# Performance work log

Hardware: AMD Instinct MI355X
Metric: run time of the kernel (lower is better)

Reference implementation:

```python
import jax, jax.numpy as jnp
import numpy as np

N, M, D, H = 256, 1024, 512, 512


def setup_inputs() -> dict:
    key = jax.random.key(0)
    k1, k2, k3, k4 = jax.random.split(key, 4)
    scale = 1.0 / np.sqrt(D)
    return {
        "embeddings": jax.random.normal(k1, (N, D), dtype=jnp.float32),
        "support_tensors": jax.random.normal(k2, (M, D), dtype=jnp.float32),
        "W1": jax.random.normal(k3, (D, H), dtype=jnp.float32) * scale,
        "b1": jnp.zeros((H,), dtype=jnp.float32),
        "W2": jax.random.normal(k4, (H, 1), dtype=jnp.float32) * (1.0 / np.sqrt(H)),
        "b2": jnp.zeros((1,), dtype=jnp.float32),
    }


def reference(embeddings, support_tensors, W1, b1, W2, b2):
    # SupportLayer.call: tile queries x support set into all N*M pairs,
    # apply pairwise kernel (siamese head: sigmoid(MLP(|a - b|))),
    # reshape back to similarity matrix [N, M].
    # Broadcasting replaces the explicit tf.tile / reshape.
    diff = jnp.abs(embeddings[:, None, :] - support_tensors[None, :, :])  # [N, M, D]
    h = jax.nn.relu(jnp.einsum("nmd,dh->nmh", diff, W1) + b1)             # [N, M, H]
    logits = jnp.einsum("nmh,ho->nmo", h, W2)[..., 0] + b2[0]             # [N, M]
    return jax.nn.sigmoid(logits)
```

## Files before the change

kernel.cpp:

```cpp
#include <hip/hip_runtime.h>
#include <hip/hip_bf16.h>

#define N_Q 256
#define M_S 1024
#define DD 512
#define HH 512

typedef __attribute__((ext_vector_type(8))) short short8;
typedef __attribute__((ext_vector_type(8))) __bf16 bf16x8;
typedef __attribute__((ext_vector_type(16))) float f32x16;
typedef __attribute__((ext_vector_type(2))) __bf16 bf16x2;

union U8 { short8 s; bf16x8 b; };

__device__ __forceinline__ unsigned short f2bf(float f) {
  unsigned int u = __float_as_uint(f);
  u += 0x7FFFu + ((u >> 16) & 1u);
  return (unsigned short)(u >> 16);
}

__device__ __forceinline__ short8 pack8(const float* d) {
#if defined(__has_builtin) && __has_builtin(__builtin_amdgcn_cvt_pk_bf16_f32)
  short8 r;
#pragma unroll
  for (int i = 0; i < 4; ++i) {
    union { bf16x2 v; short s[2]; } u;
    u.v = __builtin_amdgcn_cvt_pk_bf16_f32(d[2 * i], d[2 * i + 1]);
    r[2 * i] = u.s[0];
    r[2 * i + 1] = u.s[1];
  }
  return r;
#else
  short8 r;
#pragma unroll
  for (int i = 0; i < 8; ++i) r[i] = (short)f2bf(d[i]);
  return r;
#endif
}

__device__ __forceinline__ short8 packdiff(float4 e0, float4 e1, float4 s0, float4 s1) {
  float d[8];
  d[0] = fabsf(e0.x - s0.x); d[1] = fabsf(e0.y - s0.y);
  d[2] = fabsf(e0.z - s0.z); d[3] = fabsf(e0.w - s0.w);
  d[4] = fabsf(e1.x - s1.x); d[5] = fabsf(e1.y - s1.y);
  d[6] = fabsf(e1.z - s1.z); d[7] = fabsf(e1.w - s1.w);
  return pack8(d);
}

__global__ __launch_bounds__(512) void prep_w1s(const float* __restrict__ W1,
                                                unsigned short* __restrict__ w1s) {
  const int f = blockIdx.x;
  const int kc = f >> 4, h32 = f & 15;
  const int l = threadIdx.x & 63, j = threadIdx.x >> 6;
  const int h = h32 * 32 + (l & 31);
  const int k = kc * 16 + (l >> 5) * 8 + j;
  w1s[f * 512 + l * 8 + j] = f2bf(W1[k * HH + h]);
}

__global__ __launch_bounds__(512, 4) void support_kernel(
    const float* __restrict__ emb, const float* __restrict__ sup,
    const unsigned short* __restrict__ w1s, const float* __restrict__ b1,
    const float* __restrict__ W2, const float* __restrict__ b2,
    float* __restrict__ out) {
  __shared__ short8 As16[64 * 64];

  const int tid = threadIdx.x;
  const int lane = tid & 63;
  const int wid = tid >> 6;
  const int l31 = lane & 31;
  const int khalf = lane >> 5;

  const int m0 = blockIdx.x * 16;
  const int n0 = blockIdx.y * 4;

  const int c = tid & 63;
  const int rg = tid >> 6;
  const int nl = rg >> 1;
  const int mq = rg & 1;

  const unsigned short* bb = w1s + (wid * 2) * 512 + lane * 8;
  U8 b[3][2];
#pragma unroll
  for (int tj = 0; tj < 2; ++tj) {
    b[0][tj].s = *(const short8*)(bb + (0 * 16 + tj) * 512);
    b[1][tj].s = *(const short8*)(bb + (1 * 16 + tj) * 512);
  }

  {
    const float* ep = emb + (n0 + nl) * DD + c * 8;
    const float4 e0 = *(const float4*)ep;
    const float4 e1 = *(const float4*)(ep + 4);
    const float* sbase = sup + (m0 + mq * 8) * DD + c * 8;
#pragma unroll
    for (int j = 0; j < 8; ++j) {
      const float4 s0 = *(const float4*)(sbase + j * DD);
      const float4 s1 = *(const float4*)(sbase + j * DD + 4);
      const int p = rg * 8 + j;
      As16[p * 64 + (c ^ j)] = packdiff(e0, e1, s0, s1);
    }
  }
  __syncthreads();

  const int ar0 = (0 + l31) * 64;
  const int ar1 = (32 + l31) * 64;
  const int ax = l31 & 7;

  f32x16 acc[2][2] = {};
  U8 a[2][2];
  a[0][0].s = As16[ar0 + (khalf ^ ax)];
  a[0][1].s = As16[ar1 + (khalf ^ ax)];

#pragma unroll
  for (int ks = 0; ks < 32; ++ks) {
    const int cur = ks & 1;
    if (ks < 31) {
      const int cc = ((ks + 1) * 2 + khalf) ^ ax;
      a[cur ^ 1][0].s = As16[ar0 + cc];
      a[cur ^ 1][1].s = As16[ar1 + cc];
    }
    if (ks + 2 < 32) {
#pragma unroll
      for (int tj = 0; tj < 2; ++tj)
        b[(ks + 2) % 3][tj].s = *(const short8*)(bb + ((ks + 2) * 16 + tj) * 512);
    }
#pragma unroll
    for (int am = 0; am < 2; ++am)
#pragma unroll
      for (int tj = 0; tj < 2; ++tj)
        acc[am][tj] = __builtin_amdgcn_mfma_f32_32x32x16_bf16(
            a[cur][am].b, b[ks % 3][tj].b, acc[am][tj], 0, 0, 0);
  }

  float b1v[2], w2v[2];
#pragma unroll
  for (int tj = 0; tj < 2; ++tj) {
    const int h = (wid * 2 + tj) * 32 + l31;
    b1v[tj] = b1[h];
    w2v[tj] = W2[h];
  }
  __syncthreads();
  float* psums = (float*)As16;
#pragma unroll
  for (int am = 0; am < 2; ++am) {
#pragma unroll
    for (int r = 0; r < 16; ++r) {
      float s = fmaxf(acc[am][0][r] + b1v[0], 0.f) * w2v[0] +
                fmaxf(acc[am][1][r] + b1v[1], 0.f) * w2v[1];
      s += __shfl_xor(s, 1, 64);
      s += __shfl_xor(s, 2, 64);
      s += __shfl_xor(s, 4, 64);
      s += __shfl_xor(s, 8, 64);
      s += __shfl_xor(s, 16, 64);
      if (l31 == 0) {
        const int row32 = (r & 3) + 8 * (r >> 2) + 4 * khalf;
        psums[(am * 32 + row32) * 8 + wid] = s;
      }
    }
  }
  __syncthreads();
  if (tid < 64) {
    float t = b2[0];
#pragma unroll
    for (int w = 0; w < 8; ++w) t += psums[tid * 8 + w];
    out[(n0 + (tid >> 4)) * M_S + m0 + (tid & 15)] = 1.f / (1.f + __expf(-t));
  }
}

extern "C" void kernel_launch(void* const* d_in, const int* in_sizes, int n_in,
                              void* d_out, int out_size, void* d_ws, size_t ws_size,
                              hipStream_t stream) {
  const float* emb = (const float*)d_in[0];
  const float* sup = (const float*)d_in[1];
  const float* W1  = (const float*)d_in[2];
  const float* b1  = (const float*)d_in[3];
  const float* W2  = (const float*)d_in[4];
  const float* b2  = (const float*)d_in[5];
  float* out = (float*)d_out;
  unsigned short* w1s = (unsigned short*)d_ws;

  prep_w1s<<<512, 512, 0, stream>>>(W1, w1s);
  support_kernel<<<dim3(M_S / 16, N_Q / 4), 512, 0, stream>>>(
      emb, sup, w1s, b1, W2, b2, out);
}
```

Before: 230.6 us.

## Split hidden dim across grid z, enlarge pair tile, accumulate logits atomically

The support kernel now tiles 128 pairs (8 queries x 16 supports) per block with waves split 2x4 over pairs and hidden units. The hidden dimension is split across two blocks in grid z, and the partial logits are combined with atomicAdd into a zeroed output. A separate finalize kernel then applies bias and sigmoid. The diff tile is built in two K halves so LDS stays the same size, and the W1 prep kernel is vectorised to write short8. The aim is more reuse of W1 fragments per pair and fewer W1 reads per pair. The cost is an added memset, an extra launch, atomics and a second barrier in the K loop.

```diff
diff --git a/kernel.cpp b/kernel.cpp
--- a/kernel.cpp
+++ b/kernel.cpp
@@ -49,36 +49,36 @@
 
 __global__ __launch_bounds__(512) void prep_w1s(const float* __restrict__ W1,
                                                 unsigned short* __restrict__ w1s) {
-  const int f = blockIdx.x;
+  const int f = blockIdx.x * 8 + (threadIdx.x >> 6);
+  const int l = threadIdx.x & 63;
   const int kc = f >> 4, h32 = f & 15;
-  const int l = threadIdx.x & 63, j = threadIdx.x >> 6;
   const int h = h32 * 32 + (l & 31);
-  const int k = kc * 16 + (l >> 5) * 8 + j;
-  w1s[f * 512 + l * 8 + j] = f2bf(W1[k * HH + h]);
+  const int kb = kc * 16 + (l >> 5) * 8;
+  short8 v;
+#pragma unroll
+  for (int j = 0; j < 8; ++j) v[j] = (short)f2bf(W1[(kb + j) * HH + h]);
+  *(short8*)(w1s + f * 512 + l * 8) = v;
 }
 
 __global__ __launch_bounds__(512, 4) void support_kernel(
     const float* __restrict__ emb, const float* __restrict__ sup,
     const unsigned short* __restrict__ w1s, const float* __restrict__ b1,
-    const float* __restrict__ W2, const float* __restrict__ b2,
-    float* __restrict__ out) {
-  __shared__ short8 As16[64 * 64];
+    const float* __restrict__ W2, float* __restrict__ out) {
+  __shared__ short8 As16[128 * 32];
 
   const int tid = threadIdx.x;
   const int lane = tid & 63;
   const int wid = tid >> 6;
+  const int wm = wid & 1;
+  const int wh = wid >> 1;
   const int l31 = lane & 31;
   const int khalf = lane >> 5;
 
   const int m0 = blockIdx.x * 16;
-  const int n0 = blockIdx.y * 4;
-
-  const int c = tid & 63;
-  const int rg = tid >> 6;
-  const int nl = rg >> 1;
-  const int mq = rg & 1;
-
-  const unsigned short* bb = w1s + (wid * 2) * 512 + lane * 8;
+  const int n0 = blockIdx.y * 8;
+  const int hz = blockIdx.z;
+
+  const unsigned short* bb = w1s + (hz * 8 + wh * 2) * 512 + lane * 8;
   U8 b[3][2];
 #pragma unroll
   for (int tj = 0; tj < 2; ++tj) {
@@ -86,55 +86,67 @@
     b[1][tj].s = *(const short8*)(bb + (1 * 16 + tj) * 512);
   }
 
-  {
-    const float* ep = emb + (n0 + nl) * DD + c * 8;
-    const float4 e0 = *(const float4*)ep;
-    const float4 e1 = *(const float4*)(ep + 4);
-    const float* sbase = sup + (m0 + mq * 8) * DD + c * 8;
-#pragma unroll
-    for (int j = 0; j < 8; ++j) {
-      const float4 s0 = *(const float4*)(sbase + j * DD);
-      const float4 s1 = *(const float4*)(sbase + j * DD + 4);
-      const int p = rg * 8 + j;
-      As16[p * 64 + (c ^ j)] = packdiff(e0, e1, s0, s1);
-    }
-  }
-  __syncthreads();
-
-  const int ar0 = (0 + l31) * 64;
-  const int ar1 = (32 + l31) * 64;
+  const int c = tid & 31;
+  const int rg = tid >> 5;
+  const int nl = rg >> 1;
+  const int mq = rg & 1;
+  const float* ep_ = emb + (n0 + nl) * DD + c * 8;
+  const float* sp_ = sup + (m0 + mq * 8) * DD + c * 8;
+
+  const int ar0 = (wm * 64 + l31) * 32;
+  const int ar1 = (wm * 64 + 32 + l31) * 32;
   const int ax = l31 & 7;
 
   f32x16 acc[2][2] = {};
   U8 a[2][2];
-  a[0][0].s = As16[ar0 + (khalf ^ ax)];
-  a[0][1].s = As16[ar1 + (khalf ^ ax)];
-
-#pragma unroll
-  for (int ks = 0; ks < 32; ++ks) {
-    const int cur = ks & 1;
-    if (ks < 31) {
-      const int cc = ((ks + 1) * 2 + khalf) ^ ax;
-      a[cur ^ 1][0].s = As16[ar0 + cc];
-      a[cur ^ 1][1].s = As16[ar1 + cc];
+
+#pragma unroll
+  for (int kh = 0; kh < 2; ++kh) {
+    if (kh) __syncthreads();
+    {
+      const float4 e0 = *(const float4*)(ep_ + kh * 256);
+      const float4 e1 = *(const float4*)(ep_ + kh * 256 + 4);
+#pragma unroll
+      for (int j = 0; j < 8; ++j) {
+        const float* sp = sp_ + j * DD + kh * 256;
+        const float4 s0 = *(const float4*)sp;
+        const float4 s1 = *(const float4*)(sp + 4);
+        const int p = nl * 16 + mq * 8 + j;
+        As16[p * 32 + (c ^ j)] = packdiff(e0, e1, s0, s1);
+      }
     }
-    if (ks + 2 < 32) {
-#pragma unroll
-      for (int tj = 0; tj < 2; ++tj)
-        b[(ks + 2) % 3][tj].s = *(const short8*)(bb + ((ks + 2) * 16 + tj) * 512);
+    __syncthreads();
+
+    a[0][0].s = As16[ar0 + (khalf ^ ax)];
+    a[0][1].s = As16[ar1 + (khalf ^ ax)];
+
+#pragma unroll
+    for (int ks = 0; ks < 16; ++ks) {
+      const int gks = kh * 16 + ks;
+      const int cur = ks & 1;
+      if (ks < 15) {
+        const int cc = ((ks + 1) * 2 + khalf) ^ ax;
+        a[cur ^ 1][0].s = As16[ar0 + cc];
+        a[cur ^ 1][1].s = As16[ar1 + cc];
+      }
+      if (gks + 2 < 32) {
+#pragma unroll
+        for (int tj = 0; tj < 2; ++tj)
+          b[(gks + 2) % 3][tj].s = *(const short8*)(bb + ((gks + 2) * 16 + tj) * 512);
+      }
+#pragma unroll
+      for (int am = 0; am < 2; ++am)
+#pragma unroll
+        for (int tj = 0; tj < 2; ++tj)
+          acc[am][tj] = __builtin_amdgcn_mfma_f32_32x32x16_bf16(
+              a[cur][am].b, b[gks % 3][tj].b, acc[am][tj], 0, 0, 0);
     }
-#pragma unroll
-    for (int am = 0; am < 2; ++am)
-#pragma unroll
-      for (int tj = 0; tj < 2; ++tj)
-        acc[am][tj] = __builtin_amdgcn_mfma_f32_32x32x16_bf16(
-            a[cur][am].b, b[ks % 3][tj].b, acc[am][tj], 0, 0, 0);
   }
 
   float b1v[2], w2v[2];
 #pragma unroll
   for (int tj = 0; tj < 2; ++tj) {
-    const int h = (wid * 2 + tj) * 32 + l31;
+    const int h = hz * 256 + (wh * 2 + tj) * 32 + l31;
     b1v[tj] = b1[h];
     w2v[tj] = W2[h];
   }
@@ -153,17 +165,23 @@
       s += __shfl_xor(s, 16, 64);
       if (l31 == 0) {
         const int row32 = (r & 3) + 8 * (r >> 2) + 4 * khalf;
-        psums[(am * 32 + row32) * 8 + wid] = s;
+        psums[(wm * 64 + am * 32 + row32) * 4 + wh] = s;
       }
     }
   }
   __syncthreads();
-  if (tid < 64) {
-    float t = b2[0];
-#pragma unroll
-    for (int w = 0; w < 8; ++w) t += psums[tid * 8 + w];
-    out[(n0 + (tid >> 4)) * M_S + m0 + (tid & 15)] = 1.f / (1.f + __expf(-t));
-  }
+  if (tid < 128) {
+    const float v = psums[tid * 4] + psums[tid * 4 + 1] +
+                    psums[tid * 4 + 2] + psums[tid * 4 + 3];
+    atomicAdd(out + (n0 + (tid >> 4)) * M_S + m0 + (tid & 15), v);
+  }
+}
+
+__global__ __launch_bounds__(256) void logits_finalize(float* __restrict__ out,
+                                                       const float* __restrict__ b2) {
+  const int i = blockIdx.x * 256 + threadIdx.x;
+  const float t = out[i] + b2[0];
+  out[i] = 1.f / (1.f + __expf(-t));
 }
 
 extern "C" void kernel_launch(void* const* d_in, const int* in_sizes, int n_in,
@@ -178,7 +196,9 @@
   float* out = (float*)d_out;
   unsigned short* w1s = (unsigned short*)d_ws;
 
-  prep_w1s<<<512, 512, 0, stream>>>(W1, w1s);
-  support_kernel<<<dim3(M_S / 16, N_Q / 4), 512, 0, stream>>>(
-      emb, sup, w1s, b1, W2, b2, out);
-}
+  prep_w1s<<<64, 512, 0, stream>>>(W1, w1s);
+  hipMemsetAsync(d_out, 0, (size_t)N_Q * M_S * sizeof(float), stream);
+  support_kernel<<<dim3(M_S / 16, N_Q / 8, 2), 512, 0, stream>>>(
+      emb, sup, w1s, b1, W2, out);
+  logits_finalize<<<(N_Q * M_S) / 256, 256, 0, stream>>>(out, b2);
+}
```

Result: slower. 253.3 us (+9.8%).
